# Optimization experiments

Measured on AMD Instinct MI355X. Metric: run time of the kernel, lower is better.

The kernel has to match this reference:

```python
import jax, jax.numpy as jnp
import numpy as np

V, E, H, B, S, T, NE, NC = 50000, 300, 150, 64, 16, 48, 100001, 300


def bigru(x, Wih, Whh, bih, bhh):
    # x: [T, N, D]; PyTorch GRU cell math, bidirectional -> [T, N, 2H]
    outs = []
    for d in range(2):
        def step(h, xt, d=d):
            gi = xt @ Wih[d].T + bih[d]
            gh = h @ Whh[d].T + bhh[d]
            ir, iz, inn = jnp.split(gi, 3, axis=-1)
            hr, hz, hn = jnp.split(gh, 3, axis=-1)
            r = jax.nn.sigmoid(ir + hr)
            z = jax.nn.sigmoid(iz + hz)
            n = jnp.tanh(inn + r * hn)
            h2 = (1.0 - z) * n + z * h
            return h2, h2
        h0 = jnp.zeros((x.shape[1], Whh.shape[-1]), x.dtype)
        _, hs = jax.lax.scan(step, h0, x, reverse=(d == 1))
        outs.append(hs)
    return jnp.concatenate(outs, axis=-1)


def attend(hs, W, b, ctx):
    # hs: [T, N, G]; softmax attention over time axis
    u = jnp.tanh(jnp.einsum('tng,hg->tnh', hs, W) + b)
    a = jax.nn.softmax(jnp.einsum('tnh,h->tn', u, ctx), axis=0)
    return jnp.einsum('tn,tng->ng', a, hs)


def cos_sim(a, c, eps=1e-8):
    # a: [B, D], c: [B, K, D] -> [B, K]  (torch.cosine_similarity semantics)
    num = jnp.einsum('bd,bkd->bk', a, c)
    den = jnp.linalg.norm(a, axis=-1, keepdims=True) * jnp.linalg.norm(c, axis=-1)
    return num / jnp.maximum(den, eps)


def setup_inputs() -> dict:
    key = jax.random.key(0)
    ks = jax.random.split(key, 20)
    nrm = lambda k, s: (jax.random.normal(k, s, jnp.float32) * 0.05)
    return {
        'docs': jax.random.randint(ks[0], (B, S, T), 0, V),
        'sens': jax.random.randint(ks[1], (B,), 0, S),
        'candidates': jax.random.randint(ks[2], (B, 1, NC), 0, NE),
        'idx': jax.random.randint(ks[3], (B,), 1, NC + 1),  # 1-based gold id
        'word_emb': nrm(ks[4], (V, E)),
        'ent_emb': nrm(ks[5], (NE, E)),
        'Wih_w': nrm(ks[6], (2, 3 * H, E)),
        'Whh_w': nrm(ks[7], (2, 3 * H, H)),
        'bih_w': jnp.zeros((2, 3 * H), jnp.float32),
        'bhh_w': jnp.zeros((2, 3 * H), jnp.float32),
        'attW_w': nrm(ks[8], (2 * H, 2 * H)),
        'attb_w': jnp.zeros((2 * H,), jnp.float32),
        'ctx_w': nrm(ks[9], (2 * H,)),
        'Wih_s': nrm(ks[10], (2, 3 * H, 2 * H)),
        'Whh_s': nrm(ks[11], (2, 3 * H, H)),
        'bih_s': jnp.zeros((2, 3 * H), jnp.float32),
        'bhh_s': jnp.zeros((2, 3 * H), jnp.float32),
        'attW_s': nrm(ks[12], (2 * H, 2 * H)),
        'attb_s': jnp.zeros((2 * H,), jnp.float32),
        'ctx_s': nrm(ks[13], (2 * H,)),
        'linW': nrm(ks[14], (NC, 2 * NC)),
        'linb': jnp.zeros((NC,), jnp.float32),
    }


def reference(docs, sens, candidates, idx, word_emb, ent_emb,
              Wih_w, Whh_w, bih_w, bhh_w, attW_w, attb_w, ctx_w,
              Wih_s, Whh_s, bih_s, bhh_s, attW_s, attb_s, ctx_s,
              linW, linb):
    b, s, t = docs.shape
    # ---- word-level encoder over every sentence at once ----
    x = word_emb[docs]                              # [B,S,T,E]
    x = x.transpose(2, 0, 1, 3).reshape(t, b * s, E)  # [T, B*S, E]
    hs = bigru(x, Wih_w, Whh_w, bih_w, bhh_w)       # [T, B*S, 2H]
    sent_vec = attend(hs, attW_w, attb_w, ctx_w)    # [B*S, 2H]
    sent_vec = sent_vec.reshape(b, s, 2 * H)        # output_per_sen.permute(1,0,2)
    output_sen = sent_vec[jnp.arange(b), sens]      # [B, 2H] mention sentence
    # ---- sentence-level encoder ----
    xs = sent_vec.transpose(1, 0, 2)                # [S, B, 2H]
    hss = bigru(xs, Wih_s, Whh_s, bih_s, bhh_s)     # [S, B, 2H]
    output_doc = attend(hss, attW_s, attb_s, ctx_s)  # [B, 2H]
    # ---- batched cosine similarity against candidate entity embeddings ----
    can = ent_emb[candidates[:, 0]]                 # [B, NC, E]
    sim_total = jnp.concatenate([cos_sim(output_sen, can), cos_sim(output_doc, can)], axis=1)  # [B, 2*NC]
    score = sim_total @ linW.T + linb               # [B, NC]
    score_gold = score[jnp.arange(b), idx - 1]      # [B]
    max_index = jnp.argmax(score, axis=1)           # [B]
    return (score_gold, score, max_index)
```

## Files before the change

### kernel.cpp

```cpp
#include <hip/hip_runtime.h>
#include <hip/hip_bf16.h>
#include <math.h>

#define B_  64
#define S_  16
#define T_  48
#define E_  300
#define H_  150
#define G_  300
#define NC_ 300
#define NW_ (B_*S_)
#define RW_ (T_*NW_)
#define RS_ (S_*B_)
#define GST 960

typedef __attribute__((ext_vector_type(8))) short bf16x8;
typedef __attribute__((ext_vector_type(4))) float f32x4;

__device__ __forceinline__ float sigm(float x){ return 1.0f/(1.0f+__expf(-x)); }

__device__ __forceinline__ ushort f2bf_rne(float x){
  uint u = __float_as_uint(x);
  return (ushort)((u + 0x7FFFu + ((u>>16)&1u)) >> 16);
}

__global__ __launch_bounds__(256) void prep_whh_kernel(
    const float* __restrict__ Whh, float* __restrict__ Wblk){
  int idx = blockIdx.x*256 + threadIdx.x;
  if (idx >= 2*38*450*4) return;
  int k  = idx & 3;
  int j  = (idx >> 2) % 450;
  int e4 = (idx >> 2) / 450 % 38;
  int d  = idx / (38*450*4);
  int e  = e4*4 + k;
  Wblk[idx] = (e < 150) ? Whh[((size_t)d*450 + j)*150 + e] : 0.f;
}

__global__ __launch_bounds__(256) void prep_whh_v5(
    const float* __restrict__ Whh, float* __restrict__ W5){
  int idx = blockIdx.x*256 + threadIdx.x;
  if (idx >= 2*3*13*225*8) return;
  int kk = idx & 3;
  int r1 = idx >> 2;
  int c  = r1 & 1;
  int r2 = r1 >> 1;
  int j2 = r2 % 225;
  int r3 = r2 / 225;
  int e4 = r3 % 13;
  int r4 = r3 / 13;
  int kh = r4 % 3;
  int d  = r4 / 3;
  int j  = j2*2 + c;
  int kg = (kh*13 + e4)*4 + kk;
  W5[idx] = (kg < 150) ? Whh[((size_t)d*450 + j)*150 + kg] : 0.f;
}

__global__ __launch_bounds__(128) void split_w_gen(
    const float* __restrict__ W, ushort* __restrict__ Whi,
    ushort* __restrict__ Wlo, int R, int C, int Cp){
  int j = blockIdx.x;
  for (int k = threadIdx.x; k < Cp; k += 128){
    float x = (j < R && k < C) ? W[(size_t)j*C + k] : 0.f;
    ushort hb = f2bf_rne(x);
    float hf = __uint_as_float(((uint)hb)<<16);
    Whi[(size_t)j*Cp + k] = hb;
    Wlo[(size_t)j*Cp + k] = f2bf_rne(x - hf);
  }
}

__global__ __launch_bounds__(256,3) void gi_mfma_v2(
    const int* __restrict__ docs, const float* __restrict__ emb,
    const ushort* __restrict__ Whi, const ushort* __restrict__ Wlo,
    const float* __restrict__ bih, float* __restrict__ gi){
  __shared__ __align__(16) ushort Bhi[2][16*328];
  __shared__ __align__(16) ushort Blo[2][16*328];
  __shared__ __align__(16) float  Cst[64*68];
  __shared__ int toks[64];
  int tid = threadIdx.x;
  int gr0 = blockIdx.x * 64;
  int t  = gr0 >> 10;
  int n0 = gr0 & 1023;
  if (tid < 64) toks[tid] = docs[(n0 + tid)*T_ + t];
  uint4 pb[5];
#pragma unroll
  for (int i=0;i<5;i++){
    int c = tid + i*256;
    int half = (c >= 640) ? 1 : 0; int cc = c - half*640;
    int row = cc/40, o16 = cc - row*40;
    const ushort* src = half ? Wlo : Whi;
    pb[i] = *(const uint4*)&src[(size_t)row*320 + o16*8];
  }
  __syncthreads();
  int w = tid >> 6, L = tid & 63;
  int lrow = L & 15, lseg = L >> 4;
  const float* aptr = emb + (size_t)toks[w*16 + lrow]*300;
  bf16x8 ah[10], al[10];
#pragma unroll
  for (int ks=0; ks<10; ks++){
    int k0 = ks*32 + lseg*8;
    float x[8];
    if (k0 + 8 <= 300){
      float4 v0 = *(const float4*)&aptr[k0];
      float4 v1 = *(const float4*)&aptr[k0+4];
      x[0]=v0.x; x[1]=v0.y; x[2]=v0.z; x[3]=v0.w;
      x[4]=v1.x; x[5]=v1.y; x[6]=v1.z; x[7]=v1.w;
    } else {
#pragma unroll
      for (int u=0;u<8;u++) x[u] = (k0+u < 300) ? aptr[k0+u] : 0.f;
    }
#pragma unroll
    for (int u=0;u<8;u++){
      ushort hb = f2bf_rne(x[u]);
      float lo = x[u] - __uint_as_float(((uint)hb)<<16);
      ah[ks][u] = (short)hb;
      al[ks][u] = (short)f2bf_rne(lo);
    }
  }
#pragma unroll
  for (int i=0;i<5;i++){
    int c = tid + i*256;
    int half = (c >= 640) ? 1 : 0; int cc = c - half*640;
    int row = cc/40, o16 = cc - row*40;
    ushort* dst = half ? Blo[0] : Bhi[0];
    *(uint4*)&dst[row*328 + o16*8] = pb[i];
  }
  __syncthreads();
  int buf = 0;
  int bfb = lrow*328 + lseg*8;
  int rl0 = w*16 + lseg*4;
  f32x4 acc4[4];
  for (int g = 0; g < 14; ++g){
#pragma unroll
    for (int q = 0; q < 4; ++q){
      int nt = g*4 + q;
#pragma unroll
      for (int i=0;i<5;i++){
        int c = tid + i*256;
        int half = (c >= 640) ? 1 : 0; int cc = c - half*640;
        int row = cc/40, o16 = cc - row*40;
        const ushort* src = half ? Wlo : Whi;
        pb[i] = *(const uint4*)&src[(size_t)((nt+1)*16 + row)*320 + o16*8];
      }
      f32x4 acc = {0.f, 0.f, 0.f, 0.f};
#pragma unroll
      for (int ks=0; ks<10; ks++){
        bf16x8 bh = *(const bf16x8*)&Bhi[buf][bfb + ks*32];
        bf16x8 bl = *(const bf16x8*)&Blo[buf][bfb + ks*32];
        acc = __builtin_amdgcn_mfma_f32_16x16x32_bf16(ah[ks], bh, acc, 0, 0, 0);
        acc = __builtin_amdgcn_mfma_f32_16x16x32_bf16(ah[ks], bl, acc, 0, 0, 0);
        acc = __builtin_amdgcn_mfma_f32_16x16x32_bf16(al[ks], bh, acc, 0, 0, 0);
      }
      acc4[q] = acc;
#pragma unroll
      for (int i=0;i<5;i++){
        int c = tid + i*256;
        int half = (c >= 640) ? 1 : 0; int cc = c - half*640;
        int row = cc/40, o16 = cc - row*40;
        ushort* dst = half ? Blo[buf^1] : Bhi[buf^1];
        *(uint4*)&dst[row*328 + o16*8] = pb[i];
      }
      __syncthreads();
      buf ^= 1;
    }
#pragma unroll
    for (int q = 0; q < 4; ++q){
#pragma unroll
      for (int r = 0; r < 4; ++r)
        Cst[(rl0 + r)*68 + q*16 + lrow] = acc4[q][r];
    }
    __syncthreads();
#pragma unroll
    for (int i = 0; i < 4; ++i){
      int idxc = tid + i*256;
      int row = idxc >> 4, c4 = idxc & 15;
      int colb = g*64 + c4*4;
      float4 v = *(float4*)&Cst[row*68 + c4*4];
      float4 bb = *(const float4*)&bih[colb];
      v.x += bb.x; v.y += bb.y; v.z += bb.z; v.w += bb.w;
      *(float4*)&gi[(size_t)(gr0 + row)*GST + colb] = v;
    }
    __syncthreads();
  }
  {
    f32x4 acc = {0.f, 0.f, 0.f, 0.f};
#pragma unroll
    for (int ks=0; ks<10; ks++){
      bf16x8 bh = *(const bf16x8*)&Bhi[buf][bfb + ks*32];
      bf16x8 bl = *(const bf16x8*)&Blo[buf][bfb + ks*32];
      acc = __builtin_amdgcn_mfma_f32_16x16x32_bf16(ah[ks], bh, acc, 0, 0, 0);
      acc = __builtin_amdgcn_mfma_f32_16x16x32_bf16(ah[ks], bl, acc, 0, 0, 0);
      acc = __builtin_amdgcn_mfma_f32_16x16x32_bf16(al[ks], bh, acc, 0, 0, 0);
    }
    int col = 896 + lrow;
    if (col < 900){
      float bb = bih[col];
#pragma unroll
      for (int r=0;r<4;r++)
        gi[(size_t)(gr0 + rl0 + r)*GST + col] = acc[r] + bb;
    }
  }
}

__global__ __launch_bounds__(256,3) void att_mfma_kernel(
    const float* __restrict__ hs, const ushort* __restrict__ Whi,
    const ushort* __restrict__ Wlo, const float* __restrict__ bias,
    const float* __restrict__ ctx, float* __restrict__ score, int Rtot){
  __shared__ __align__(16) ushort Bhi[2][16*328];
  __shared__ __align__(16) ushort Blo[2][16*328];
  int tid = threadIdx.x;
  int r0 = blockIdx.x * 64;
  uint4 pb[5];
#pragma unroll
  for (int i=0;i<5;i++){
    int c = tid + i*256;
    int half = (c >= 640) ? 1 : 0; int cc = c - half*640;
    int row = cc/40, o16 = cc - row*40;
    const ushort* src = half ? Wlo : Whi;
    pb[i] = *(const uint4*)&src[(size_t)row*320 + o16*8];
  }
  int w = tid >> 6, L = tid & 63;
  int lrow = L & 15, lseg = L >> 4;
  int arow = r0 + w*16 + lrow;
  bool avalid = arow < Rtot;
  const float* aptr = hs + (size_t)(avalid ? arow : 0)*300;
  bf16x8 ah[10], al[10];
#pragma unroll
  for (int ks=0; ks<10; ks++){
    int k0 = ks*32 + lseg*8;
    float x[8];
    if (avalid && k0 + 8 <= 300){
      float4 v0 = *(const float4*)&aptr[k0];
      float4 v1 = *(const float4*)&aptr[k0+4];
      x[0]=v0.x; x[1]=v0.y; x[2]=v0.z; x[3]=v0.w;
      x[4]=v1.x; x[5]=v1.y; x[6]=v1.z; x[7]=v1.w;
    } else {
#pragma unroll
      for (int u=0;u<8;u++) x[u] = (avalid && k0+u < 300) ? aptr[k0+u] : 0.f;
    }
#pragma unroll
    for (int u=0;u<8;u++){
      ushort hb = f2bf_rne(x[u]);
      float lo = x[u] - __uint_as_float(((uint)hb)<<16);
      ah[ks][u] = (short)hb;
      al[ks][u] = (short)f2bf_rne(lo);
    }
  }
#pragma unroll
  for (int i=0;i<5;i++){
    int c = tid + i*256;
    int half = (c >= 640) ? 1 : 0; int cc = c - half*640;
    int row = cc/40, o16 = cc - row*40;
    ushort* dst = half ? Blo[0] : Bhi[0];
    *(uint4*)&dst[row*328 + o16*8] = pb[i];
  }
  __syncthreads();
  int buf = 0;
  int bfb = lrow*328 + lseg*8;
  float part[4] = {0.f,0.f,0.f,0.f};
  for (int nt = 0; nt < 19; ++nt){
    if (nt < 18){
#pragma unroll
      for (int i=0;i<5;i++){
        int c = tid + i*256;
        int half = (c >= 640) ? 1 : 0; int cc = c - half*640;
        int row = cc/40, o16 = cc - row*40;
        const ushort* src = half ? Wlo : Whi;
        pb[i] = *(const uint4*)&src[(size_t)((nt+1)*16 + row)*320 + o16*8];
      }
    }
    f32x4 acc = {0.f, 0.f, 0.f, 0.f};
#pragma unroll
    for (int ks=0; ks<10; ks++){
      bf16x8 bh = *(const bf16x8*)&Bhi[buf][bfb + ks*32];
      bf16x8 bl = *(const bf16x8*)&Blo[buf][bfb + ks*32];
      acc = __builtin_amdgcn_mfma_f32_16x16x32_bf16(ah[ks], bh, acc, 0, 0, 0);
      acc = __builtin_amdgcn_mfma_f32_16x16x32_bf16(ah[ks], bl, acc, 0, 0, 0);
      acc = __builtin_amdgcn_mfma_f32_16x16x32_bf16(al[ks], bh, acc, 0, 0, 0);
    }
    int col = nt*16 + lrow;
    if (col < 300){
      float bb = bias[col], cx = ctx[col];
#pragma unroll
      for (int r=0;r<4;r++) part[r] += cx * tanhf(acc[r] + bb);
    }
    if (nt < 18){
#pragma unroll
      for (int i=0;i<5;i++){
        int c = tid + i*256;
        int half = (c >= 640) ? 1 : 0; int cc = c - half*640;
        int row = cc/40, o16 = cc - row*40;
        ushort* dst = half ? Blo[buf^1] : Bhi[buf^1];
        *(uint4*)&dst[row*328 + o16*8] = pb[i];
      }
    }
    __syncthreads();
    buf ^= 1;
  }
#pragma unroll
  for (int off=1; off<16; off<<=1){
#pragma unroll
    for (int r=0;r<4;r++) part[r] += __shfl_xor(part[r], off);
  }
  if (lrow == 0){
    int rbase = r0 + w*16 + lseg*4;
#pragma unroll
    for (int r=0;r<4;r++)
      if (rbase + r < Rtot) score[rbase + r] = part[r];
  }
}

__global__ __launch_bounds__(256) void sent_gi_kernel(
    const float* __restrict__ sv, const float* __restrict__ Wih,
    const float* __restrict__ bih, float* __restrict__ gi){
  __shared__ float A[16][G_];
  int r0 = blockIdx.x * 16;
  int s  = r0 >> 6;
  int bb_ = r0 & 63;
  for (int idx = threadIdx.x; idx < 16*75; idx += 256){
    int row = idx / 75, e4 = idx - row*75;
    *(float4*)&A[row][e4*4] =
        *(const float4*)&sv[(((size_t)(bb_+row))*S_ + s)*G_ + e4*4];
  }
  __syncthreads();
  int q = threadIdx.x;
  if (q >= 225) return;
  int j0 = q*4;
  const float4* w0 = (const float4*)(Wih + (size_t)(j0  )*G_);
  const float4* w1 = (const float4*)(Wih + (size_t)(j0+1)*G_);
  const float4* w2 = (const float4*)(Wih + (size_t)(j0+2)*G_);
  const float4* w3 = (const float4*)(Wih + (size_t)(j0+3)*G_);
  float acc[16][4];
#pragma unroll
  for (int i=0;i<16;i++){ acc[i][0]=0.f; acc[i][1]=0.f; acc[i][2]=0.f; acc[i][3]=0.f; }
  for (int e4=0; e4<75; e4++){
    float4 b0=w0[e4], b1=w1[e4], b2=w2[e4], b3=w3[e4];
#pragma unroll
    for (int i=0;i<16;i++){
      float4 av = *(const float4*)&A[i][e4*4];
      acc[i][0] += av.x*b0.x + av.y*b0.y + av.z*b0.z + av.w*b0.w;
      acc[i][1] += av.x*b1.x + av.y*b1.y + av.z*b1.z + av.w*b1.w;
      acc[i][2] += av.x*b2.x + av.y*b2.y + av.z*b2.z + av.w*b2.w;
      acc[i][3] += av.x*b3.x + av.y*b3.y + av.z*b3.z + av.w*b3.w;
    }
  }
  float4 bb = *(const float4*)&bih[j0];
#pragma unroll
  for (int i=0;i<16;i++){
    float4 o4;
    o4.x = acc[i][0]+bb.x; o4.y = acc[i][1]+bb.y;
    o4.z = acc[i][2]+bb.z; o4.w = acc[i][3]+bb.w;
    *(float4*)&gi[((size_t)(s*B_) + bb_ + i)*GST + j0] = o4;
  }
}

__global__ __launch_bounds__(768,3) void gru_scan_v5(
    const float* __restrict__ gi, const float* __restrict__ W5,
    const float* __restrict__ bhh, float* __restrict__ hs,
    int T, int N){
  int d  = blockIdx.y;
  int n0 = blockIdx.x * 8;
  __shared__ float hl[2][8][160];
  __shared__ float ghp[3][8][452];
  int tid = threadIdx.x;
  for (int idx = tid; idx < 2*8*160; idx += 768) (&hl[0][0][0])[idx] = 0.f;
  bool gact = tid < 675;
  int j2 = gact ? tid % 225 : 0;
  int kh = gact ? tid / 225 : 0;
  float4 Wr[13][2];
  {
    const float4* wb = (const float4*)(W5 + (size_t)(d*3 + kh)*13*225*8);
#pragma unroll
    for (int e4=0;e4<13;e4++){
      Wr[e4][0] = wb[(e4*225 + j2)*2 + 0];
      Wr[e4][1] = wb[(e4*225 + j2)*2 + 1];
    }
  }
#pragma unroll
  for (int e4=0;e4<13;e4++){
    asm volatile("" : "+v"(Wr[e4][0].x), "+v"(Wr[e4][0].y),
                      "+v"(Wr[e4][0].z), "+v"(Wr[e4][0].w));
    asm volatile("" : "+v"(Wr[e4][1].x), "+v"(Wr[e4][1].y),
                      "+v"(Wr[e4][1].z), "+v"(Wr[e4][1].w));
  }
  float b0 = 0.f, b1 = 0.f;
  if (gact && kh == 0){
    b0 = bhh[d*450 + 2*j2];
    b1 = bhh[d*450 + 2*j2 + 1];
  }
  int i0 = tid/150,        h0 = tid - i0*150;
  int u1 = tid + 768;
  int i1 = u1/150,         h1 = u1 - i1*150;
  bool e1 = u1 < 1200;
  int buf = 0;
  __syncthreads();
  for (int step = 0; step < T; ++step){
    int t = d ? (T-1-step) : step;
    const float* gib = gi + ((size_t)t*N + n0)*GST + d*450;
    float p0r = gib[(size_t)i0*GST + h0];
    float p0z = gib[(size_t)i0*GST + 150 + h0];
    float p0n = gib[(size_t)i0*GST + 300 + h0];
    float p1r=0.f, p1z=0.f, p1n=0.f;
    if (e1){
      p1r = gib[(size_t)i1*GST + h1];
      p1z = gib[(size_t)i1*GST + 150 + h1];
      p1n = gib[(size_t)i1*GST + 300 + h1];
    }
    if (gact){
      float a0[8], a1[8];
#pragma unroll
      for (int i=0;i<8;i++){ a0[i]=0.f; a1[i]=0.f; }
#pragma unroll
      for (int e4=0;e4<13;e4++){
        float4 w0 = Wr[e4][0], w1 = Wr[e4][1];
#pragma unroll
        for (int i=0;i<8;i++){
          float4 hv = *(const float4*)&hl[buf][i][(kh*13+e4)*4];
          a0[i] += w0.x*hv.x + w0.y*hv.y + w0.z*hv.z + w0.w*hv.w;
          a1[i] += w1.x*hv.x + w1.y*hv.y + w1.z*hv.z + w1.w*hv.w;
        }
      }
#pragma unroll
      for (int i=0;i<8;i++){
        float2 v; v.x = a0[i] + b0; v.y = a1[i] + b1;
        *(float2*)&ghp[kh][i][2*j2] = v;
      }
    }
    __syncthreads();
    {
      float ghr = ghp[0][i0][h0]     + ghp[1][i0][h0]     + ghp[2][i0][h0];
      float ghz = ghp[0][i0][150+h0] + ghp[1][i0][150+h0] + ghp[2][i0][150+h0];
      float ghn = ghp[0][i0][300+h0] + ghp[1][i0][300+h0] + ghp[2][i0][300+h0];
      float hold = hl[buf][i0][h0];
      float r  = sigm(p0r + ghr);
      float z  = sigm(p0z + ghz);
      float nn = tanhf(p0n + r*ghn);
      float h2 = (1.f - z)*nn + z*hold;
      hl[buf^1][i0][h0] = h2;
      hs[((size_t)t*N + n0 + i0)*G_ + d*H_ + h0] = h2;
    }
    if (e1){
      float ghr = ghp[0][i1][h1]     + ghp[1][i1][h1]     + ghp[2][i1][h1];
      float ghz = ghp[0][i1][150+h1] + ghp[1][i1][150+h1] + ghp[2][i1][150+h1];
      float ghn = ghp[0][i1][300+h1] + ghp[1][i1][300+h1] + ghp[2][i1][300+h1];
      float hold = hl[buf][i1][h1];
      float r  = sigm(p1r + ghr);
      float z  = sigm(p1z + ghz);
      float nn = tanhf(p1n + r*ghn);
      float h2 = (1.f - z)*nn + z*hold;
      hl[buf^1][i1][h1] = h2;
      hs[((size_t)t*N + n0 + i1)*G_ + d*H_ + h1] = h2;
    }
    buf ^= 1;
    __syncthreads();
  }
}

template<int R>
__global__ __launch_bounds__(512,2) void gru_scan_v4(
    const float* __restrict__ gi, const float* __restrict__ Wblk,
    const float* __restrict__ bhh, float* __restrict__ hs,
    int T, int N){
  int d  = blockIdx.y;
  int n0 = blockIdx.x * R;
  __shared__ float hl[2][R][152];
  __shared__ float gh[R][452];
  int tid = threadIdx.x;
  for (int idx = tid; idx < 2*R*152; idx += 512) (&hl[0][0][0])[idx] = 0.f;
  bool jact = tid < 450;
  bool hact = tid < 150;
  float4 Wr[38];
  float bj = 0.f;
  {
    const float4* Wb4 = (const float4*)(Wblk + (size_t)d*38*1800);
    int jj = jact ? tid : 0;
#pragma unroll
    for (int e4 = 0; e4 < 38; ++e4) Wr[e4] = Wb4[e4*450 + jj];
    if (jact) bj = bhh[d*450 + tid];
  }
  float hreg[R];
#pragma unroll
  for (int i=0;i<R;i++) hreg[i] = 0.f;
  int buf = 0;
  __syncthreads();
  for (int step = 0; step < T; ++step){
    int t = d ? (T-1-step) : step;
    const float* gib = gi + ((size_t)t*N + n0)*GST + d*450;
    float pre[R][3];
    if (hact){
#pragma unroll
      for (int i=0;i<R;i++){
        pre[i][0] = gib[(size_t)i*GST + tid];
        pre[i][1] = gib[(size_t)i*GST + 150 + tid];
        pre[i][2] = gib[(size_t)i*GST + 300 + tid];
      }
    }
    if (jact){
      float acc[R];
#pragma unroll
      for (int i=0;i<R;i++) acc[i] = 0.f;
#pragma unroll
      for (int e4 = 0; e4 < 38; ++e4){
        float4 w = Wr[e4];
#pragma unroll
        for (int i=0;i<R;i++){
          float4 hv = *(const float4*)&hl[buf][i][e4*4];
          acc[i] += w.x*hv.x + w.y*hv.y + w.z*hv.z + w.w*hv.w;
        }
      }
#pragma unroll
      for (int i=0;i<R;i++) gh[i][tid] = acc[i] + bj;
    }
    __syncthreads();
    if (hact){
#pragma unroll
      for (int i=0;i<R;i++){
        float r  = sigm(pre[i][0] + gh[i][tid]);
        float z  = sigm(pre[i][1] + gh[i][150+tid]);
        float nn = tanhf(pre[i][2] + r*gh[i][300+tid]);
        float h2 = (1.f - z)*nn + z*hreg[i];
        hreg[i] = h2;
        hl[buf^1][i][tid] = h2;
        hs[((size_t)t*N + n0 + i)*G_ + d*H_ + tid] = h2;
      }
    }
    buf ^= 1;
    __syncthreads();
  }
}

__global__ __launch_bounds__(256) void att_combine_kernel(
    const float* __restrict__ score, const float* __restrict__ hs,
    float* __restrict__ out, int T, int N){
  int n = blockIdx.x;
  __shared__ float wa[64];
  if (threadIdx.x < T) wa[threadIdx.x] = score[threadIdx.x*N + n];
  __syncthreads();
  float m = -1e30f;
  for (int t=0;t<T;t++) m = fmaxf(m, wa[t]);
  float den = 0.f;
  for (int t=0;t<T;t++) den += __expf(wa[t]-m);
  float inv = 1.f/den;
  __syncthreads();
  if (threadIdx.x < T) wa[threadIdx.x] = __expf(wa[threadIdx.x]-m)*inv;
  __syncthreads();
  for (int g = threadIdx.x; g < G_; g += 256){
    float acc = 0.f;
    for (int t=0;t<T;t++) acc += wa[t] * hs[((size_t)t*N+n)*G_ + g];
    out[(size_t)n*G_ + g] = acc;
  }
}

__global__ __launch_bounds__(256) void cossim_kernel(
    const int* __restrict__ cand, const int* __restrict__ sens,
    const float* __restrict__ ent, const float* __restrict__ sv,
    const float* __restrict__ odoc, float* __restrict__ sim){
  int w = (blockIdx.x*256 + threadIdx.x) >> 6;
  int lane = threadIdx.x & 63;
  if (w >= B_*NC_) return;
  int b = w / NC_, k = w - b*NC_;
  const float* c  = ent + (size_t)cand[b*NC_ + k]*E_;
  const float* a1 = sv  + ((size_t)b*S_ + sens[b])*G_;
  const float* a2 = odoc + (size_t)b*G_;
  float d1=0.f,d2=0.f,cc=0.f,n1=0.f,n2=0.f;
  for (int e = lane; e < E_; e += 64){
    float cv=c[e], v1=a1[e], v2=a2[e];
    d1+=v1*cv; d2+=v2*cv; cc+=cv*cv; n1+=v1*v1; n2+=v2*v2;
  }
  for (int off=32; off; off>>=1){
    d1+=__shfl_xor(d1,off); d2+=__shfl_xor(d2,off); cc+=__shfl_xor(cc,off);
    n1+=__shfl_xor(n1,off); n2+=__shfl_xor(n2,off);
  }
  if (lane == 0){
    float nc = sqrtf(cc);
    sim[(size_t)b*600 + k]       = d1 / fmaxf(sqrtf(n1)*nc, 1e-8f);
    sim[(size_t)b*600 + 300 + k] = d2 / fmaxf(sqrtf(n2)*nc, 1e-8f);
  }
}

__global__ __launch_bounds__(256) void final_kernel(
    const float* __restrict__ sim, const float* __restrict__ linW,
    const float* __restrict__ linb, const int* __restrict__ idx,
    float* __restrict__ out){
  int b = blockIdx.x;
  __shared__ float ss[600];
  __shared__ float sc[300];
  __shared__ float bv[256];
  __shared__ int   bi[256];
  for (int j = threadIdx.x; j < 600; j += 256) ss[j] = sim[(size_t)b*600 + j];
  __syncthreads();
  float bestv = -1e30f; int besti = 0;
  for (int i = threadIdx.x; i < 300; i += 256){
    const float4* wr = (const float4*)(linW + (size_t)i*600);
    float acc = linb[i];
    for (int j4=0; j4<150; j4++){
      float4 w = wr[j4];
      int j = j4*4;
      acc += w.x*ss[j] + w.y*ss[j+1] + w.z*ss[j+2] + w.w*ss[j+3];
    }
    sc[i] = acc;
    out[64 + (size_t)b*300 + i] = acc;
    if (acc > bestv){ bestv = acc; besti = i; }
  }
  bv[threadIdx.x] = bestv; bi[threadIdx.x] = besti;
  __syncthreads();
  for (int s=128; s; s>>=1){
    if (threadIdx.x < s){
      float ov = bv[threadIdx.x+s]; int oi = bi[threadIdx.x+s];
      if (ov > bv[threadIdx.x] || (ov == bv[threadIdx.x] && oi < bi[threadIdx.x])){
        bv[threadIdx.x] = ov; bi[threadIdx.x] = oi;
      }
    }
    __syncthreads();
  }
  if (threadIdx.x == 0){
    out[b] = sc[idx[b]-1];
    out[64 + 64*300 + b] = (float)bi[0];
  }
}

extern "C" void kernel_launch(void* const* d_in, const int* in_sizes, int n_in,
                              void* d_out, int out_size, void* d_ws, size_t ws_size,
                              hipStream_t stream){
  const int*   docs  = (const int*)d_in[0];
  const int*   sens  = (const int*)d_in[1];
  const int*   cand  = (const int*)d_in[2];
  const int*   idx   = (const int*)d_in[3];
  const float* wemb  = (const float*)d_in[4];
  const float* eemb  = (const float*)d_in[5];
  const float* Wih_w = (const float*)d_in[6];
  const float* Whh_w = (const float*)d_in[7];
  const float* bih_w = (const float*)d_in[8];
  const float* bhh_w = (const float*)d_in[9];
  const float* attW_w= (const float*)d_in[10];
  const float* attb_w= (const float*)d_in[11];
  const float* ctx_w = (const float*)d_in[12];
  const float* Wih_s = (const float*)d_in[13];
  const float* Whh_s = (const float*)d_in[14];
  const float* bih_s = (const float*)d_in[15];
  const float* bhh_s = (const float*)d_in[16];
  const float* attW_s= (const float*)d_in[17];
  const float* attb_s= (const float*)d_in[18];
  const float* ctx_s = (const float*)d_in[19];
  const float* linW  = (const float*)d_in[20];
  const float* linb  = (const float*)d_in[21];

  float* ws = (float*)d_ws;
  size_t off = 0;
  float* gi_w    = ws + off; off += (size_t)T_*NW_*GST;
  float* hs_w    = ws + off; off += (size_t)T_*NW_*G_;
  float* score_w = ws + off; off += (size_t)T_*NW_;
  float* sv      = ws + off; off += (size_t)NW_*G_;
  float* hs_s    = ws + off; off += (size_t)S_*B_*G_;
  float* score_s = ws + off; off += (size_t)S_*B_;
  float* odoc    = ws + off; off += (size_t)B_*G_;
  float* sim     = ws + off; off += (size_t)B_*600;
  float* Wblk_s  = ws + off; off += (size_t)2*38*450*4;
  float* W5_w    = ws + off; off += (size_t)2*3*13*225*8;
  ushort* Whi    = (ushort*)(ws + off); off += (size_t)912*320/2;
  ushort* Wlo    = (ushort*)(ws + off); off += (size_t)912*320/2;
  ushort* WAhi   = (ushort*)(ws + off); off += (size_t)304*320/2;
  ushort* WAlo   = (ushort*)(ws + off); off += (size_t)304*320/2;
  ushort* WShi   = (ushort*)(ws + off); off += (size_t)304*320/2;
  ushort* WSlo   = (ushort*)(ws + off); off += (size_t)304*320/2;
  float* gi_s    = gi_w;

  float* out = (float*)d_out;

  prep_whh_kernel<<<(2*38*450*4+255)/256, 256, 0, stream>>>(Whh_s, Wblk_s);
  prep_whh_v5<<<(2*3*13*225*8+255)/256, 256, 0, stream>>>(Whh_w, W5_w);
  split_w_gen<<<912, 128, 0, stream>>>(Wih_w, Whi, Wlo, 900, 300, 320);
  split_w_gen<<<304, 128, 0, stream>>>(attW_w, WAhi, WAlo, 300, 300, 320);
  split_w_gen<<<304, 128, 0, stream>>>(attW_s, WShi, WSlo, 300, 300, 320);

  gi_mfma_v2<<<RW_/64, 256, 0, stream>>>(docs, wemb, Whi, Wlo, bih_w, gi_w);
  gru_scan_v5<<<dim3(NW_/8, 2), 768, 0, stream>>>(gi_w, W5_w, bhh_w,
                                                  hs_w, T_, NW_);
  att_mfma_kernel<<<RW_/64, 256, 0, stream>>>(hs_w, WAhi, WAlo, attb_w,
                                              ctx_w, score_w, RW_);
  att_combine_kernel<<<NW_, 256, 0, stream>>>(score_w, hs_w, sv, T_, NW_);

  sent_gi_kernel<<<RS_/16, 256, 0, stream>>>(sv, Wih_s, bih_s, gi_s);
  gru_scan_v4<2><<<dim3(B_/2, 2), 512, 0, stream>>>(gi_s, Wblk_s, bhh_s,
                                                    hs_s, S_, B_);
  att_mfma_kernel<<<RS_/64, 256, 0, stream>>>(hs_s, WShi, WSlo, attb_s,
                                              ctx_s, score_s, RS_);
  att_combine_kernel<<<B_, 256, 0, stream>>>(score_s, hs_s, odoc, S_, B_);

  cossim_kernel<<<(B_*NC_*64)/256, 256, 0, stream>>>(cand, sens, eemb, sv, odoc, sim);
  final_kernel<<<B_, 256, 0, stream>>>(sim, linW, linb, idx, out);
}
```

Before: 799.5 us.

## Move word-level GRU recurrent matmul to split-bf16 MFMA with 16-row blocks

Replaces the FP32 VALU recurrent h@Whh product in the word-level GRU scan with MFMA 16x16x32 bf16 instructions. It uses a hi/lo split (three products) to keep close to FP32 accuracy, and holds the split weights in registers. Each block now handles 16 sequences with 512 threads instead of 8 with 768, which halves the grid. The hidden state is kept as bf16 hi/lo pairs in LDS and as FP32 in registers. The aim is to cut the ALU-bound sequential matmul cost per step, at the price of a small precision change and a different occupancy and grid shape.

```diff
diff --git a/kernel.cpp b/kernel.cpp
--- a/kernel.cpp
+++ b/kernel.cpp
@@ -36,23 +36,18 @@
   Wblk[idx] = (e < 150) ? Whh[((size_t)d*450 + j)*150 + e] : 0.f;
 }
 
-__global__ __launch_bounds__(256) void prep_whh_v5(
-    const float* __restrict__ Whh, float* __restrict__ W5){
+__global__ __launch_bounds__(256) void prep_whh_mfma(
+    const float* __restrict__ Whh, ushort* __restrict__ Bsh,
+    ushort* __restrict__ Bsl){
   int idx = blockIdx.x*256 + threadIdx.x;
-  if (idx >= 2*3*13*225*8) return;
-  int kk = idx & 3;
-  int r1 = idx >> 2;
-  int c  = r1 & 1;
-  int r2 = r1 >> 1;
-  int j2 = r2 % 225;
-  int r3 = r2 / 225;
-  int e4 = r3 % 13;
-  int r4 = r3 / 13;
-  int kh = r4 % 3;
-  int d  = r4 / 3;
-  int j  = j2*2 + c;
-  int kg = (kh*13 + e4)*4 + kk;
-  W5[idx] = (kg < 150) ? Whh[((size_t)d*450 + j)*150 + kg] : 0.f;
+  if (idx >= 2*512*160) return;
+  int k = idx % 160;
+  int j = (idx / 160) % 512;
+  int d = idx / (512*160);
+  float x = (j < 450 && k < 150) ? Whh[((size_t)d*450 + j)*150 + k] : 0.f;
+  ushort hb = f2bf_rne(x);
+  Bsh[idx] = hb;
+  Bsl[idx] = f2bf_rne(x - __uint_as_float(((uint)hb)<<16));
 }
 
 __global__ __launch_bounds__(128) void split_w_gen(
@@ -353,104 +348,100 @@
   }
 }
 
-__global__ __launch_bounds__(768,3) void gru_scan_v5(
-    const float* __restrict__ gi, const float* __restrict__ W5,
-    const float* __restrict__ bhh, float* __restrict__ hs,
-    int T, int N){
+__global__ __launch_bounds__(512,2) void gru_mfma(
+    const float* __restrict__ gi, const ushort* __restrict__ Bsh,
+    const ushort* __restrict__ Bsl, const float* __restrict__ bhh,
+    float* __restrict__ hs, int T, int N){
+  __shared__ __align__(16) ushort Ahi[16*168];
+  __shared__ __align__(16) ushort Alo[16*168];
+  __shared__ float gh[16*468];
+  int tid = threadIdx.x;
   int d  = blockIdx.y;
-  int n0 = blockIdx.x * 8;
-  __shared__ float hl[2][8][160];
-  __shared__ float ghp[3][8][452];
-  int tid = threadIdx.x;
-  for (int idx = tid; idx < 2*8*160; idx += 768) (&hl[0][0][0])[idx] = 0.f;
-  bool gact = tid < 675;
-  int j2 = gact ? tid % 225 : 0;
-  int kh = gact ? tid / 225 : 0;
-  float4 Wr[13][2];
+  int n0 = blockIdx.x * 16;
+  for (int i = tid; i < 16*168; i += 512){ Ahi[i] = 0; Alo[i] = 0; }
+  int wv = tid >> 6, L = tid & 63;
+  int lrow = L & 15, lseg = L >> 4;
+  bf16x8 Bh[4][5], Bl[4][5];
   {
-    const float4* wb = (const float4*)(W5 + (size_t)(d*3 + kh)*13*225*8);
-#pragma unroll
-    for (int e4=0;e4<13;e4++){
-      Wr[e4][0] = wb[(e4*225 + j2)*2 + 0];
-      Wr[e4][1] = wb[(e4*225 + j2)*2 + 1];
-    }
-  }
-#pragma unroll
-  for (int e4=0;e4<13;e4++){
-    asm volatile("" : "+v"(Wr[e4][0].x), "+v"(Wr[e4][0].y),
-                      "+v"(Wr[e4][0].z), "+v"(Wr[e4][0].w));
-    asm volatile("" : "+v"(Wr[e4][1].x), "+v"(Wr[e4][1].y),
-                      "+v"(Wr[e4][1].z), "+v"(Wr[e4][1].w));
-  }
-  float b0 = 0.f, b1 = 0.f;
-  if (gact && kh == 0){
-    b0 = bhh[d*450 + 2*j2];
-    b1 = bhh[d*450 + 2*j2 + 1];
-  }
-  int i0 = tid/150,        h0 = tid - i0*150;
-  int u1 = tid + 768;
-  int i1 = u1/150,         h1 = u1 - i1*150;
-  bool e1 = u1 < 1200;
-  int buf = 0;
+    const ushort* bh_ = Bsh + (size_t)d*512*160;
+    const ushort* bl_ = Bsl + (size_t)d*512*160;
+#pragma unroll
+    for (int q=0;q<4;q++){
+      int row = (wv + q*8)*16 + lrow;
+#pragma unroll
+      for (int ks=0;ks<5;ks++){
+        Bh[q][ks] = *(const bf16x8*)&bh_[(size_t)row*160 + lseg*8 + ks*32];
+        Bl[q][ks] = *(const bf16x8*)&bl_[(size_t)row*160 + lseg*8 + ks*32];
+      }
+    }
+  }
+  int erow[5], eh[5];
+  float bb_r[5], bb_z[5], bb_n[5], hold[5];
+#pragma unroll
+  for (int r=0;r<5;r++){
+    int e = tid + r*512;
+    bool v = e < 2400;
+    int e2 = v ? e : 0;
+    erow[r] = e2 / 150; eh[r] = e2 % 150;
+    bb_r[r] = v ? bhh[d*450 + eh[r]]        : 0.f;
+    bb_z[r] = v ? bhh[d*450 + 150 + eh[r]]  : 0.f;
+    bb_n[r] = v ? bhh[d*450 + 300 + eh[r]]  : 0.f;
+    hold[r] = 0.f;
+  }
   __syncthreads();
   for (int step = 0; step < T; ++step){
     int t = d ? (T-1-step) : step;
+    bf16x8 Ah[5], Al[5];
+#pragma unroll
+    for (int ks=0;ks<5;ks++){
+      Ah[ks] = *(const bf16x8*)&Ahi[lrow*168 + lseg*8 + ks*32];
+      Al[ks] = *(const bf16x8*)&Alo[lrow*168 + lseg*8 + ks*32];
+    }
+#pragma unroll
+    for (int q=0;q<4;q++){
+      int nt = wv + q*8;
+      if (nt < 29){
+        f32x4 acc = {0.f,0.f,0.f,0.f};
+#pragma unroll
+        for (int ks=0;ks<5;ks++){
+          acc = __builtin_amdgcn_mfma_f32_16x16x32_bf16(Ah[ks], Bh[q][ks], acc, 0,0,0);
+          acc = __builtin_amdgcn_mfma_f32_16x16x32_bf16(Ah[ks], Bl[q][ks], acc, 0,0,0);
+          acc = __builtin_amdgcn_mfma_f32_16x16x32_bf16(Al[ks], Bh[q][ks], acc, 0,0,0);
+        }
+        int col = nt*16 + lrow;
+#pragma unroll
+        for (int r=0;r<4;r++)
+          gh[(lseg*4 + r)*468 + col] = acc[r];
+      }
+    }
     const float* gib = gi + ((size_t)t*N + n0)*GST + d*450;
-    float p0r = gib[(size_t)i0*GST + h0];
-    float p0z = gib[(size_t)i0*GST + 150 + h0];
-    float p0n = gib[(size_t)i0*GST + 300 + h0];
-    float p1r=0.f, p1z=0.f, p1n=0.f;
-    if (e1){
-      p1r = gib[(size_t)i1*GST + h1];
-      p1z = gib[(size_t)i1*GST + 150 + h1];
-      p1n = gib[(size_t)i1*GST + 300 + h1];
-    }
-    if (gact){
-      float a0[8], a1[8];
-#pragma unroll
-      for (int i=0;i<8;i++){ a0[i]=0.f; a1[i]=0.f; }
-#pragma unroll
-      for (int e4=0;e4<13;e4++){
-        float4 w0 = Wr[e4][0], w1 = Wr[e4][1];
-#pragma unroll
-        for (int i=0;i<8;i++){
-          float4 hv = *(const float4*)&hl[buf][i][(kh*13+e4)*4];
-          a0[i] += w0.x*hv.x + w0.y*hv.y + w0.z*hv.z + w0.w*hv.w;
-          a1[i] += w1.x*hv.x + w1.y*hv.y + w1.z*hv.z + w1.w*hv.w;
-        }
-      }
-#pragma unroll
-      for (int i=0;i<8;i++){
-        float2 v; v.x = a0[i] + b0; v.y = a1[i] + b1;
-        *(float2*)&ghp[kh][i][2*j2] = v;
-      }
-    }
-    __syncthreads();
-    {
-      float ghr = ghp[0][i0][h0]     + ghp[1][i0][h0]     + ghp[2][i0][h0];
-      float ghz = ghp[0][i0][150+h0] + ghp[1][i0][150+h0] + ghp[2][i0][150+h0];
-      float ghn = ghp[0][i0][300+h0] + ghp[1][i0][300+h0] + ghp[2][i0][300+h0];
-      float hold = hl[buf][i0][h0];
-      float r  = sigm(p0r + ghr);
-      float z  = sigm(p0z + ghz);
-      float nn = tanhf(p0n + r*ghn);
-      float h2 = (1.f - z)*nn + z*hold;
-      hl[buf^1][i0][h0] = h2;
-      hs[((size_t)t*N + n0 + i0)*G_ + d*H_ + h0] = h2;
-    }
-    if (e1){
-      float ghr = ghp[0][i1][h1]     + ghp[1][i1][h1]     + ghp[2][i1][h1];
-      float ghz = ghp[0][i1][150+h1] + ghp[1][i1][150+h1] + ghp[2][i1][150+h1];
-      float ghn = ghp[0][i1][300+h1] + ghp[1][i1][300+h1] + ghp[2][i1][300+h1];
-      float hold = hl[buf][i1][h1];
-      float r  = sigm(p1r + ghr);
-      float z  = sigm(p1z + ghz);
-      float nn = tanhf(p1n + r*ghn);
-      float h2 = (1.f - z)*nn + z*hold;
-      hl[buf^1][i1][h1] = h2;
-      hs[((size_t)t*N + n0 + i1)*G_ + d*H_ + h1] = h2;
-    }
-    buf ^= 1;
+    float pr[5], pz[5], pn[5];
+#pragma unroll
+    for (int r=0;r<5;r++){
+      if (tid + r*512 < 2400){
+        const float* g0 = gib + (size_t)erow[r]*GST + eh[r];
+        pr[r] = g0[0]; pz[r] = g0[150]; pn[r] = g0[300];
+      }
+    }
+    __syncthreads();
+#pragma unroll
+    for (int r=0;r<5;r++){
+      if (tid + r*512 < 2400){
+        int row = erow[r], h = eh[r];
+        float ghr = gh[row*468 + h];
+        float ghz = gh[row*468 + 150 + h];
+        float ghn = gh[row*468 + 300 + h];
+        float rr = sigm(pr[r] + ghr + bb_r[r]);
+        float zz = sigm(pz[r] + ghz + bb_z[r]);
+        float nn = tanhf(pn[r] + rr*(ghn + bb_n[r]));
+        float h2 = (1.f - zz)*nn + zz*hold[r];
+        hold[r] = h2;
+        ushort hb = f2bf_rne(h2);
+        Ahi[row*168 + h] = hb;
+        Alo[row*168 + h] = f2bf_rne(h2 - __uint_as_float(((uint)hb)<<16));
+        hs[((size_t)t*N + n0 + row)*G_ + d*H_ + h] = h2;
+      }
+    }
     __syncthreads();
   }
 }
@@ -655,26 +646,27 @@
   float* odoc    = ws + off; off += (size_t)B_*G_;
   float* sim     = ws + off; off += (size_t)B_*600;
   float* Wblk_s  = ws + off; off += (size_t)2*38*450*4;
-  float* W5_w    = ws + off; off += (size_t)2*3*13*225*8;
   ushort* Whi    = (ushort*)(ws + off); off += (size_t)912*320/2;
   ushort* Wlo    = (ushort*)(ws + off); off += (size_t)912*320/2;
   ushort* WAhi   = (ushort*)(ws + off); off += (size_t)304*320/2;
   ushort* WAlo   = (ushort*)(ws + off); off += (size_t)304*320/2;
   ushort* WShi   = (ushort*)(ws + off); off += (size_t)304*320/2;
   ushort* WSlo   = (ushort*)(ws + off); off += (size_t)304*320/2;
+  ushort* Bsh    = (ushort*)(ws + off); off += (size_t)2*512*160/2;
+  ushort* Bsl    = (ushort*)(ws + off); off += (size_t)2*512*160/2;
   float* gi_s    = gi_w;
 
   float* out = (float*)d_out;
 
   prep_whh_kernel<<<(2*38*450*4+255)/256, 256, 0, stream>>>(Whh_s, Wblk_s);
-  prep_whh_v5<<<(2*3*13*225*8+255)/256, 256, 0, stream>>>(Whh_w, W5_w);
+  prep_whh_mfma<<<(2*512*160+255)/256, 256, 0, stream>>>(Whh_w, Bsh, Bsl);
   split_w_gen<<<912, 128, 0, stream>>>(Wih_w, Whi, Wlo, 900, 300, 320);
   split_w_gen<<<304, 128, 0, stream>>>(attW_w, WAhi, WAlo, 300, 300, 320);
   split_w_gen<<<304, 128, 0, stream>>>(attW_s, WShi, WSlo, 300, 300, 320);
 
   gi_mfma_v2<<<RW_/64, 256, 0, stream>>>(docs, wemb, Whi, Wlo, bih_w, gi_w);
-  gru_scan_v5<<<dim3(NW_/8, 2), 768, 0, stream>>>(gi_w, W5_w, bhh_w,
-                                                  hs_w, T_, NW_);
+  gru_mfma<<<dim3(NW_/16, 2), 512, 0, stream>>>(gi_w, Bsh, Bsl, bhh_w,
+                                                hs_w, T_, NW_);
   att_mfma_kernel<<<RW_/64, 256, 0, stream>>>(hs_w, WAhi, WAlo, attb_w,
                                               ctx_w, score_w, RW_);
   att_combine_kernel<<<NW_, 256, 0, stream>>>(score_w, hs_w, sv, T_, NW_);
```

Measured after the change: 867.3 us. +8.5%, slower.
